# Optimization experiments

Measured on AMD Instinct MI355X. Metric: run time of the kernel, lower is better.

## Reference

```python
import jax, jax.numpy as jnp
import numpy as np

D_MODEL, N_LAYERS, D_INNER, D_STATE, D_CONV, DT_RANK, NUM_CLASSES = 256, 4, 512, 16, 4, 16, 10
B, L = 8, 1024


def setup_inputs() -> dict:
    key = jax.random.key(0)
    ks = jax.random.split(key, 16)
    s = 0.02
    inp = {}
    inp['x'] = jax.random.normal(ks[0], (B, L, 1), jnp.float32)
    inp['input_w'] = jax.random.normal(ks[1], (D_MODEL, 1), jnp.float32) * s
    inp['input_b'] = jnp.zeros((D_MODEL,), jnp.float32)
    inp['ln_w'] = jnp.ones((N_LAYERS, D_MODEL), jnp.float32)
    inp['ln_b'] = jnp.zeros((N_LAYERS, D_MODEL), jnp.float32)
    inp['in_proj_w'] = jax.random.normal(ks[2], (N_LAYERS, 2 * D_INNER, D_MODEL), jnp.float32) * s
    inp['in_proj_b'] = jnp.zeros((N_LAYERS, 2 * D_INNER), jnp.float32)
    inp['conv_w'] = jax.random.normal(ks[3], (N_LAYERS, D_INNER, 1, D_CONV), jnp.float32) * 0.2
    inp['conv_b'] = jnp.zeros((N_LAYERS, D_INNER), jnp.float32)
    inp['x_proj_w'] = jax.random.normal(ks[4], (N_LAYERS, DT_RANK + 2 * D_STATE, D_INNER), jnp.float32) * s
    inp['dt_proj_w'] = jax.random.normal(ks[5], (N_LAYERS, D_INNER, DT_RANK), jnp.float32) * s
    inp['dt_proj_b'] = jax.random.normal(ks[6], (N_LAYERS, D_INNER), jnp.float32) * 0.1 - 4.0  # small softplus(dt)
    # canonical S4D-real init: A = [1..d_state] repeated over d_inner
    A = jnp.tile(jnp.arange(1, D_STATE + 1, dtype=jnp.float32)[None, :], (D_INNER, 1))
    inp['A_log'] = jnp.tile(jnp.log(A)[None], (N_LAYERS, 1, 1))
    inp['D'] = jnp.ones((N_LAYERS, D_INNER), jnp.float32)
    inp['out_proj_w'] = jax.random.normal(ks[7], (N_LAYERS, D_MODEL, D_INNER), jnp.float32) * s
    inp['out_proj_b'] = jnp.zeros((N_LAYERS, D_MODEL), jnp.float32)
    inp['norm_w'] = jnp.ones((D_MODEL,), jnp.float32)
    inp['norm_b'] = jnp.zeros((D_MODEL,), jnp.float32)
    inp['cls_w'] = jax.random.normal(ks[8], (NUM_CLASSES, D_MODEL), jnp.float32) * s
    inp['cls_b'] = jnp.zeros((NUM_CLASSES,), jnp.float32)
    return inp


def _layernorm(x, w, b, eps=1e-5):
    mu = jnp.mean(x, axis=-1, keepdims=True)
    var = jnp.mean(jnp.square(x - mu), axis=-1, keepdims=True)
    return (x - mu) * jax.lax.rsqrt(var + eps) * w + b


def _causal_depthwise_conv(u, w, b):
    # u: (B, L, D_inner), w: (D_inner, 1, K), causal padding K-1
    out = jax.lax.conv_general_dilated(
        u.transpose(0, 2, 1), w, window_strides=(1,), padding=[(D_CONV - 1, 0)],
        feature_group_count=D_INNER, dimension_numbers=('NCH', 'OIH', 'NCH'))
    return out.transpose(0, 2, 1) + b


def _selective_scan(u, delta, A, Bm, Cm, Dp):
    # u, delta: (B,L,Din); Bm, Cm: (B,L,N); A: (Din,N); Dp: (Din,)
    def step(h, inp):
        d_t, B_t, C_t, u_t = inp                       # (B,Din),(B,N),(B,N),(B,Din)
        dA = jnp.exp(d_t[:, :, None] * A)              # (B,Din,N)
        dBu = d_t[:, :, None] * B_t[:, None, :] * u_t[:, :, None]
        h = dA * h + dBu
        y = jnp.einsum('bdn,bn->bd', h, C_t)
        return h, y
    h0 = jnp.zeros((u.shape[0], D_INNER, D_STATE), u.dtype)
    xs = (delta.transpose(1, 0, 2), Bm.transpose(1, 0, 2), Cm.transpose(1, 0, 2), u.transpose(1, 0, 2))
    _, ys = jax.lax.scan(step, h0, xs)                 # ys: (L,B,Din)
    return ys.transpose(1, 0, 2) + u * Dp


def _mamba_layer(x, ln_w, ln_b, ipw, ipb, cw, cb, xpw, dtw, dtb, A_log, Dp, opw, opb):
    h = _layernorm(x, ln_w, ln_b)
    xz = jnp.einsum('bld,ed->ble', h, ipw) + ipb       # (B,L,2*Din)
    u, res = jnp.split(xz, 2, axis=-1)
    u = jax.nn.silu(_causal_depthwise_conv(u, cw, cb))
    x_dbl = jnp.einsum('bld,ed->ble', u, xpw)          # (B,L,dt_rank+2N)
    dt, Bm, Cm = jnp.split(x_dbl, [DT_RANK, DT_RANK + D_STATE], axis=-1)
    delta = jax.nn.softplus(jnp.einsum('blr,dr->bld', dt, dtw) + dtb)
    A = -jnp.exp(A_log)
    y = _selective_scan(u, delta, A, Bm, Cm, Dp)
    y = y * jax.nn.silu(res)
    return x + jnp.einsum('ble,de->bld', y, opw) + opb


def reference(x, input_w, input_b, ln_w, ln_b, in_proj_w, in_proj_b, conv_w, conv_b,
              x_proj_w, dt_proj_w, dt_proj_b, A_log, D, out_proj_w, out_proj_b,
              norm_w, norm_b, cls_w, cls_b):
    h = jnp.einsum('blc,dc->bld', x, input_w) + input_b   # (B,L,D_MODEL)
    for i in range(N_LAYERS):
        h = _mamba_layer(h, ln_w[i], ln_b[i], in_proj_w[i], in_proj_b[i], conv_w[i], conv_b[i],
                         x_proj_w[i], dt_proj_w[i], dt_proj_b[i], A_log[i], D[i],
                         out_proj_w[i], out_proj_b[i])
    h = _layernorm(h, norm_w, norm_b)
    pooled = jnp.mean(h, axis=1)                          # (B, D_MODEL)
    return jnp.einsum('bd,cd->bc', pooled, cls_w) + cls_b
```

## Files before the change

kernel.cpp:

```cpp
#include <hip/hip_runtime.h>
#include <hip/hip_bf16.h>
#include <math.h>

#define DM 256
#define NL 4
#define DI 512
#define DS 16
#define DC 4
#define DR 16
#define NC 10
#define NB 8
#define LL 1024
#define MR (NB*LL)
#define NCHUNK 64
#define CLEN 16

typedef __attribute__((ext_vector_type(4))) float f32x4;
typedef __attribute__((ext_vector_type(8))) short short8;

extern "C" __device__ float __ocml_native_exp2_f32(float);
__device__ __forceinline__ float exp2_f(float x) { return __ocml_native_exp2_f32(x); }
#define L2E 1.442695040888963f

__device__ __forceinline__ float silu_f(float x) {
    return x * (1.0f / (1.0f + __expf(-x)));
}
__device__ __forceinline__ float bf2f(ushort v) {
    union { unsigned u; float f; } c; c.u = ((unsigned)v) << 16; return c.f;
}
__device__ __forceinline__ ushort f2bf(float f) {
    union { float f; unsigned u; } c; c.f = f;
    unsigned lsb = (c.u >> 16) & 1;
    return (ushort)((c.u + 0x7fffu + lsb) >> 16);
}
__device__ __forceinline__ void g2lds16(const void* g, void* l) {
    __builtin_amdgcn_global_load_lds((const __attribute__((address_space(1))) void*)g,
                                     (__attribute__((address_space(3))) void*)l, 16, 0, 0);
}

#define IPW_N (NL*2*DI*DM)
#define XPW_N (NL*64*DI)
#define OPW_N (NL*DM*DI)
__global__ __launch_bounds__(256) void convert_weights_kernel(
        const float* __restrict__ ipw, const float* __restrict__ xpw,
        const float* __restrict__ opw,
        ushort* __restrict__ ipw_b, ushort* __restrict__ xpw_b, ushort* __restrict__ opw_b) {
    int t = blockIdx.x * 256 + threadIdx.x;
    if (t < IPW_N) { ipw_b[t] = f2bf(ipw[t]); return; }
    t -= IPW_N;
    if (t < XPW_N) {
        int l = t >> 15, r = (t >> 9) & 63, k = t & 511;
        xpw_b[t] = (r < 48) ? f2bf(xpw[((size_t)l * 48 + r) * DI + k]) : (ushort)0;
        return;
    }
    t -= XPW_N;
    if (t < OPW_N) opw_b[t] = f2bf(opw[t]);
}

__global__ void input_proj_kernel(const float* __restrict__ x, const float* __restrict__ w,
                                  const float* __restrict__ b, float* __restrict__ h) {
    int t = blockIdx.x * 256 + threadIdx.x;
    if (t >= MR * DM) return;
    int d = t & (DM - 1);
    int m = t >> 8;
    h[t] = x[m] * w[d] + b[d];
}

__global__ __launch_bounds__(256) void layernorm_bf16_kernel(const float* __restrict__ in,
        const float* __restrict__ w, const float* __restrict__ b, ushort* __restrict__ out) {
    int row = blockIdx.x, t = threadIdx.x;
    float v = in[row * DM + t];
    float s = v, q = v * v;
#pragma unroll
    for (int o = 32; o >= 1; o >>= 1) { s += __shfl_xor(s, o); q += __shfl_xor(q, o); }
    __shared__ float red[8];
    int wid = t >> 6;
    if ((t & 63) == 0) { red[wid] = s; red[4 + wid] = q; }
    __syncthreads();
    s = red[0] + red[1] + red[2] + red[3];
    q = red[4] + red[5] + red[6] + red[7];
    float mu = s * (1.0f / DM);
    float var = q * (1.0f / DM) - mu * mu;
    float rs = rsqrtf(var + 1e-5f);
    out[row * DM + t] = f2bf((v - mu) * rs * w[t] + b[t]);
}

template<int BM, int BN, int WM, int WN, int MODE>
__global__ __launch_bounds__(256) void mfma_gemm_kernel(
        const ushort* __restrict__ A, int lda,
        const ushort* __restrict__ W,
        const float* __restrict__ bias,
        ushort* __restrict__ Cb, float* __restrict__ Cf, int ldc, int K) {
    constexpr int FM = BM / WM / 16;
    constexpr int FN = BN / WN / 16;
    __shared__ __align__(16) char smem[(BM + BN) * 128];
    const int tid = threadIdx.x;
    const int l = tid & 63, w = tid >> 6;
    const int wr = w / WN, wc = w % WN;
    const int bm = blockIdx.x * BM, bn = blockIdx.y * BN;
    const int ldw = K;

    f32x4 acc[FM][FN] = {};

    for (int k0 = 0; k0 < K; k0 += 64) {
#pragma unroll
        for (int i = 0; i < (BM * 128 / 16) / 256; i++) {
            int lin = (i * 256 + tid) * 16;
            int q = lin ^ (((lin >> 7) & 7) << 4);
            g2lds16(A + (size_t)(bm + (q >> 7)) * lda + k0 + ((q & 127) >> 1), smem + lin);
        }
#pragma unroll
        for (int i = 0; i < (BN * 128 / 16) / 256; i++) {
            int lin = (i * 256 + tid) * 16;
            int q = lin ^ (((lin >> 7) & 7) << 4);
            g2lds16(W + (size_t)(bn + (q >> 7)) * ldw + k0 + ((q & 127) >> 1),
                    smem + BM * 128 + lin);
        }
        __syncthreads();
        const int rl = l & 15;
        const int kb0 = ((l >> 4) << 3) * 2;
#pragma unroll
        for (int kk = 0; kk < 2; kk++) {
            short8 af[FM], bfr[FN];
#pragma unroll
            for (int m = 0; m < FM; m++) {
                int off = (wr * (BM / WM) + m * 16 + rl) * 128 + kk * 64 + kb0;
                off ^= ((off >> 7) & 7) << 4;
                af[m] = *(const short8*)(smem + off);
            }
#pragma unroll
            for (int n = 0; n < FN; n++) {
                int off = (wc * (BN / WN) + n * 16 + rl) * 128 + kk * 64 + kb0;
                off ^= ((off >> 7) & 7) << 4;
                bfr[n] = *(const short8*)(smem + BM * 128 + off);
            }
#pragma unroll
            for (int m = 0; m < FM; m++)
#pragma unroll
                for (int n = 0; n < FN; n++)
                    acc[m][n] = __builtin_amdgcn_mfma_f32_16x16x32_bf16(
                        af[m], bfr[n], acc[m][n], 0, 0, 0);
        }
        __syncthreads();
    }

    const int row0 = bm + wr * (BM / WM) + ((l >> 4) << 2);
    const int col0 = bn + wc * (BN / WN) + (l & 15);
#pragma unroll
    for (int m = 0; m < FM; m++) {
#pragma unroll
        for (int n = 0; n < FN; n++) {
            int col = col0 + n * 16;
            float bv = (MODE == 1) ? 0.f : bias[col];
#pragma unroll
            for (int r = 0; r < 4; r++) {
                size_t idx = (size_t)(row0 + m * 16 + r) * ldc + col;
                float v = acc[m][n][r];
                if (MODE == 0) Cb[idx] = f2bf(v + bv);
                else Cf[idx] = v;
            }
        }
    }
}

__global__ __launch_bounds__(256) void outproj_ln_kernel(
        const ushort* __restrict__ A,
        const ushort* __restrict__ W,
        const float* __restrict__ bias,
        float* __restrict__ hres,
        const float* __restrict__ lnw, const float* __restrict__ lnb,
        ushort* __restrict__ hln) {
    constexpr int K = DI;
    __shared__ __align__(16) char smem[(32 + 256) * 128];
    const int tid = threadIdx.x;
    const int l = tid & 63, w = tid >> 6;
    const int bm = blockIdx.x * 32;

    f32x4 acc[2][4] = {};

    for (int k0 = 0; k0 < K; k0 += 64) {
        {
            int lin = tid * 16;
            int q = lin ^ (((lin >> 7) & 7) << 4);
            g2lds16(A + (size_t)(bm + (q >> 7)) * K + k0 + ((q & 127) >> 1), smem + lin);
        }
#pragma unroll
        for (int i = 0; i < 8; i++) {
            int lin = (i * 256 + tid) * 16;
            int q = lin ^ (((lin >> 7) & 7) << 4);
            g2lds16(W + (size_t)(q >> 7) * K + k0 + ((q & 127) >> 1), smem + 32 * 128 + lin);
        }
        __syncthreads();
        const int rl = l & 15;
        const int kb0 = ((l >> 4) << 3) * 2;
#pragma unroll
        for (int kk = 0; kk < 2; kk++) {
            short8 af[2], bfr[4];
#pragma unroll
            for (int m = 0; m < 2; m++) {
                int off = (m * 16 + rl) * 128 + kk * 64 + kb0;
                off ^= ((off >> 7) & 7) << 4;
                af[m] = *(const short8*)(smem + off);
            }
#pragma unroll
            for (int n = 0; n < 4; n++) {
                int off = (w * 64 + n * 16 + rl) * 128 + kk * 64 + kb0;
                off ^= ((off >> 7) & 7) << 4;
                bfr[n] = *(const short8*)(smem + 32 * 128 + off);
            }
#pragma unroll
            for (int m = 0; m < 2; m++)
#pragma unroll
                for (int n = 0; n < 4; n++)
                    acc[m][n] = __builtin_amdgcn_mfma_f32_16x16x32_bf16(
                        af[m], bfr[n], acc[m][n], 0, 0, 0);
        }
        __syncthreads();
    }

    const int r0 = (l >> 4) << 2;
    const int col0 = w * 64 + (l & 15);
    float vv[2][4][4];
    float s[2][4], q[2][4];
#pragma unroll
    for (int m = 0; m < 2; m++)
#pragma unroll
        for (int r = 0; r < 4; r++) { s[m][r] = 0.f; q[m][r] = 0.f; }
#pragma unroll
    for (int m = 0; m < 2; m++) {
#pragma unroll
        for (int n = 0; n < 4; n++) {
            int col = col0 + n * 16;
            float bv = bias[col];
#pragma unroll
            for (int r = 0; r < 4; r++) {
                int row = bm + r0 + m * 16 + r;
                float x = acc[m][n][r] + bv + hres[(size_t)row * DM + col];
                vv[m][n][r] = x;
                s[m][r] += x;
                q[m][r] += x * x;
            }
        }
    }
#pragma unroll
    for (int o = 1; o < 16; o <<= 1) {
#pragma unroll
        for (int m = 0; m < 2; m++)
#pragma unroll
            for (int r = 0; r < 4; r++) {
                s[m][r] += __shfl_xor(s[m][r], o);
                q[m][r] += __shfl_xor(q[m][r], o);
            }
    }
    float* red  = (float*)smem;
    float* redq = red + 128;
    if ((l & 15) == 0) {
#pragma unroll
        for (int m = 0; m < 2; m++)
#pragma unroll
            for (int r = 0; r < 4; r++) {
                int rl2 = r0 + m * 16 + r;
                red[rl2 * 4 + w] = s[m][r];
                redq[rl2 * 4 + w] = q[m][r];
            }
    }
    __syncthreads();
#pragma unroll
    for (int m = 0; m < 2; m++) {
        float mu[4], rs[4];
#pragma unroll
        for (int r = 0; r < 4; r++) {
            int rl2 = r0 + m * 16 + r;
            float ts = red[rl2 * 4] + red[rl2 * 4 + 1] + red[rl2 * 4 + 2] + red[rl2 * 4 + 3];
            float tq = redq[rl2 * 4] + redq[rl2 * 4 + 1] + redq[rl2 * 4 + 2] + redq[rl2 * 4 + 3];
            mu[r] = ts * (1.0f / DM);
            float var = tq * (1.0f / DM) - mu[r] * mu[r];
            rs[r] = rsqrtf(var + 1e-5f);
        }
#pragma unroll
        for (int n = 0; n < 4; n++) {
            int col = col0 + n * 16;
            float lw = lnw[col], lb = lnb[col];
#pragma unroll
            for (int r = 0; r < 4; r++) {
                int row = bm + r0 + m * 16 + r;
                hres[(size_t)row * DM + col] = vv[m][n][r];
                hln[(size_t)row * DM + col] = f2bf((vv[m][n][r] - mu[r]) * rs[r] * lw + lb);
            }
        }
    }
}

__global__ __launch_bounds__(256) void conv_silu_kernel(const ushort* __restrict__ xz,
        const float* __restrict__ cw, const float* __restrict__ cb, ushort* __restrict__ u) {
    int t = blockIdx.x * 256 + threadIdx.x;
    int d8 = (t & 63) << 3;
    int m = t >> 6;
    int l = m & (LL - 1);
    const short8 zr = {0, 0, 0, 0, 0, 0, 0, 0};
    const size_t base = (size_t)m * 1024 + d8;
    short8 r3 = *(const short8*)(xz + base);
    short8 r2 = (l >= 1) ? *(const short8*)(xz + base - 1024) : zr;
    short8 r1 = (l >= 2) ? *(const short8*)(xz + base - 2048) : zr;
    short8 r0 = (l >= 3) ? *(const short8*)(xz + base - 3072) : zr;
    short8 o;
#pragma unroll
    for (int j = 0; j < 8; j++) {
        int d = d8 + j;
        float4 w4 = *reinterpret_cast<const float4*>(&cw[d * 4]);
        float a = cb[d] + w4.w * bf2f((ushort)r3[j]);
        a += w4.z * bf2f((ushort)r2[j]);
        a += w4.y * bf2f((ushort)r1[j]);
        a += w4.x * bf2f((ushort)r0[j]);
        o[j] = (short)f2bf(silu_f(a));
    }
    *(short8*)(u + (size_t)m * DI + d8) = o;
}

__global__ __launch_bounds__(256, 4) void scan_phase1_kernel(
        const ushort* __restrict__ u, const float* __restrict__ x_dbl,
        const float* __restrict__ A_log,
        const float* __restrict__ dtw, const float* __restrict__ dtb,
        float* __restrict__ sdv, float* __restrict__ Sbuf) {
    __shared__ __align__(16) float xs[CLEN * 64];
    const int tid = threadIdx.x;
    const int bc = blockIdx.x >> 1;
    const int d = ((blockIdx.x & 1) << 8) + tid;
    const int c = bc & (NCHUNK - 1);
    const int b = bc >> 6;
    const int m0 = b * LL + c * CLEN;
    *reinterpret_cast<float4*>(&xs[tid * 4]) =
        *reinterpret_cast<const float4*>(&x_dbl[(size_t)m0 * 64 + tid * 4]);

    float Aval[DS], h[DS], wreg[DR];
#pragma unroll
    for (int q = 0; q < 4; q++) {
        float4 a4 = *reinterpret_cast<const float4*>(&A_log[d * DS + q * 4]);
        Aval[q*4+0] = -__expf(a4.x) * L2E; Aval[q*4+1] = -__expf(a4.y) * L2E;
        Aval[q*4+2] = -__expf(a4.z) * L2E; Aval[q*4+3] = -__expf(a4.w) * L2E;
        float4 w4 = *reinterpret_cast<const float4*>(&dtw[d * DR + q * 4]);
        wreg[q*4] = w4.x; wreg[q*4+1] = w4.y; wreg[q*4+2] = w4.z; wreg[q*4+3] = w4.w;
    }
    float dbv = dtb[d];
#pragma unroll
    for (int n = 0; n < DS; n++) h[n] = 0.f;
    const ushort* up = u + (size_t)m0 * DI + d;
    float sd = 0.f;
    __syncthreads();
    float uv = bf2f(up[0]);
    for (int t = 0; t < CLEN; t++) {
        float uvn = (t + 1 < CLEN) ? bf2f(up[(size_t)(t + 1) * DI]) : 0.f;
        const float* xr = &xs[t * 64];
        float4 x0 = *reinterpret_cast<const float4*>(xr);
        float4 x1 = *reinterpret_cast<const float4*>(xr + 4);
        float4 x2 = *reinterpret_cast<const float4*>(xr + 8);
        float4 x3 = *reinterpret_cast<const float4*>(xr + 12);
        float4 B0 = *reinterpret_cast<const float4*>(xr + 16);
        float4 B1 = *reinterpret_cast<const float4*>(xr + 20);
        float4 B2 = *reinterpret_cast<const float4*>(xr + 24);
        float4 B3 = *reinterpret_cast<const float4*>(xr + 28);
        float p0 = dbv + wreg[0]*x0.x + wreg[1]*x0.y + wreg[2]*x0.z + wreg[3]*x0.w;
        float p1 = wreg[4]*x1.x + wreg[5]*x1.y + wreg[6]*x1.z + wreg[7]*x1.w;
        float p2 = wreg[8]*x2.x + wreg[9]*x2.y + wreg[10]*x2.z + wreg[11]*x2.w;
        float p3 = wreg[12]*x3.x + wreg[13]*x3.y + wreg[14]*x3.z + wreg[15]*x3.w;
        float z = (p0 + p1) + (p2 + p3);
        float dv = (z > 20.0f) ? z : __logf(1.0f + __expf(z));
        sd += dv;
        float du = dv * uv;
        h[0]  = exp2_f(dv*Aval[0])  * h[0]  + du * B0.x;
        h[1]  = exp2_f(dv*Aval[1])  * h[1]  + du * B0.y;
        h[2]  = exp2_f(dv*Aval[2])  * h[2]  + du * B0.z;
        h[3]  = exp2_f(dv*Aval[3])  * h[3]  + du * B0.w;
        h[4]  = exp2_f(dv*Aval[4])  * h[4]  + du * B1.x;
        h[5]  = exp2_f(dv*Aval[5])  * h[5]  + du * B1.y;
        h[6]  = exp2_f(dv*Aval[6])  * h[6]  + du * B1.z;
        h[7]  = exp2_f(dv*Aval[7])  * h[7]  + du * B1.w;
        h[8]  = exp2_f(dv*Aval[8])  * h[8]  + du * B2.x;
        h[9]  = exp2_f(dv*Aval[9])  * h[9]  + du * B2.y;
        h[10] = exp2_f(dv*Aval[10]) * h[10] + du * B2.z;
        h[11] = exp2_f(dv*Aval[11]) * h[11] + du * B2.w;
        h[12] = exp2_f(dv*Aval[12]) * h[12] + du * B3.x;
        h[13] = exp2_f(dv*Aval[13]) * h[13] + du * B3.y;
        h[14] = exp2_f(dv*Aval[14]) * h[14] + du * B3.z;
        h[15] = exp2_f(dv*Aval[15]) * h[15] + du * B3.w;
        uv = uvn;
    }
    size_t base = ((size_t)((b * NCHUNK + c) * DI + d)) * DS;
#pragma unroll
    for (int q = 0; q < 4; q++)
        *reinterpret_cast<float4*>(&Sbuf[base + q * 4]) =
            make_float4(h[q*4], h[q*4+1], h[q*4+2], h[q*4+3]);
    sdv[(b * NCHUNK + c) * DI + d] = sd;
}

__global__ __launch_bounds__(256) void scan_phase2_kernel(
        const float* __restrict__ sdv, const float* __restrict__ A_log,
        float* __restrict__ Sbuf) {
    int gid = blockIdx.x * 256 + threadIdx.x;
    int dn = gid & (DI * DS - 1);
    int b = gid >> 13;
    int n = dn & 15, d = dn >> 4;
    float Aval = -__expf(A_log[d * DS + n]) * L2E;
    size_t idx0 = (size_t)b * NCHUNK * DI * DS + dn;
    const size_t stride = (size_t)DI * DS;
    int sb0 = b * NCHUNK * DI + d;
    float h = 0.f;
    float S0[8], sd0[8];
#pragma unroll
    for (int j = 0; j < 8; j++) {
        S0[j] = Sbuf[idx0 + (size_t)j * stride];
        sd0[j] = sdv[sb0 + j * DI];
    }
    for (int g = 0; g < 8; g++) {
        float S1[8], sd1[8];
        if (g < 7) {
            int c1 = g * 8 + 8;
#pragma unroll
            for (int j = 0; j < 8; j++) {
                S1[j] = Sbuf[idx0 + (size_t)(c1 + j) * stride];
                sd1[j] = sdv[sb0 + (c1 + j) * DI];
            }
        } else {
#pragma unroll
            for (int j = 0; j < 8; j++) { S1[j] = 0.f; sd1[j] = 0.f; }
        }
#pragma unroll
        for (int j = 0; j < 8; j++) {
            float P = exp2_f(Aval * sd0[j]);
            Sbuf[idx0 + (size_t)(g * 8 + j) * stride] = h;
            h = P * h + S0[j];
        }
#pragma unroll
        for (int j = 0; j < 8; j++) { S0[j] = S1[j]; sd0[j] = sd1[j]; }
    }
}

__global__ __launch_bounds__(256, 4) void scan_phase3_kernel(
        const ushort* __restrict__ u, const float* __restrict__ x_dbl,
        const float* __restrict__ A_log,
        const float* __restrict__ dtw, const float* __restrict__ dtb,
        const float* __restrict__ Dp, const float* __restrict__ Sbuf,
        const ushort* __restrict__ xz, ushort* __restrict__ y) {
    __shared__ __align__(16) float xs[CLEN * 64];
    const int tid = threadIdx.x;
    const int bc = blockIdx.x >> 1;
    const int d = ((blockIdx.x & 1) << 8) + tid;
    const int c = bc & (NCHUNK - 1);
    const int b = bc >> 6;
    const int m0 = b * LL + c * CLEN;
    *reinterpret_cast<float4*>(&xs[tid * 4]) =
        *reinterpret_cast<const float4*>(&x_dbl[(size_t)m0 * 64 + tid * 4]);

    float Aval[DS], h[DS], wreg[DR];
#pragma unroll
    for (int q = 0; q < 4; q++) {
        float4 a4 = *reinterpret_cast<const float4*>(&A_log[d * DS + q * 4]);
        Aval[q*4+0] = -__expf(a4.x) * L2E; Aval[q*4+1] = -__expf(a4.y) * L2E;
        Aval[q*4+2] = -__expf(a4.z) * L2E; Aval[q*4+3] = -__expf(a4.w) * L2E;
        float4 w4 = *reinterpret_cast<const float4*>(&dtw[d * DR + q * 4]);
        wreg[q*4] = w4.x; wreg[q*4+1] = w4.y; wreg[q*4+2] = w4.z; wreg[q*4+3] = w4.w;
    }
    float dbv = dtb[d];
    size_t base = ((size_t)((b * NCHUNK + c) * DI + d)) * DS;
#pragma unroll
    for (int q = 0; q < 4; q++) {
        float4 h4 = *reinterpret_cast<const float4*>(&Sbuf[base + q * 4]);
        h[q*4] = h4.x; h[q*4+1] = h4.y; h[q*4+2] = h4.z; h[q*4+3] = h4.w;
    }
    float Dval = Dp[d];
    const ushort* up = u + (size_t)m0 * DI + d;
    const ushort* rp = xz + (size_t)m0 * 1024 + 512 + d;
    ushort* yp = y + (size_t)m0 * DI + d;
    __syncthreads();
    float uv = bf2f(up[0]);
    float rv = bf2f(rp[0]);
    for (int t = 0; t < CLEN; t++) {
        float uvn = 0.f, rvn = 0.f;
        if (t + 1 < CLEN) {
            uvn = bf2f(up[(size_t)(t + 1) * DI]);
            rvn = bf2f(rp[(size_t)(t + 1) * 1024]);
        }
        const float* xr = &xs[t * 64];
        float4 x0 = *reinterpret_cast<const float4*>(xr);
        float4 x1 = *reinterpret_cast<const float4*>(xr + 4);
        float4 x2 = *reinterpret_cast<const float4*>(xr + 8);
        float4 x3 = *reinterpret_cast<const float4*>(xr + 12);
        float4 B0 = *reinterpret_cast<const float4*>(xr + 16);
        float4 B1 = *reinterpret_cast<const float4*>(xr + 20);
        float4 B2 = *reinterpret_cast<const float4*>(xr + 24);
        float4 B3 = *reinterpret_cast<const float4*>(xr + 28);
        float4 C0 = *reinterpret_cast<const float4*>(xr + 32);
        float4 C1 = *reinterpret_cast<const float4*>(xr + 36);
        float4 C2 = *reinterpret_cast<const float4*>(xr + 40);
        float4 C3 = *reinterpret_cast<const float4*>(xr + 44);
        float p0 = dbv + wreg[0]*x0.x + wreg[1]*x0.y + wreg[2]*x0.z + wreg[3]*x0.w;
        float p1 = wreg[4]*x1.x + wreg[5]*x1.y + wreg[6]*x1.z + wreg[7]*x1.w;
        float p2 = wreg[8]*x2.x + wreg[9]*x2.y + wreg[10]*x2.z + wreg[11]*x2.w;
        float p3 = wreg[12]*x3.x + wreg[13]*x3.y + wreg[14]*x3.z + wreg[15]*x3.w;
        float z = (p0 + p1) + (p2 + p3);
        float dv = (z > 20.0f) ? z : __logf(1.0f + __expf(z));
        float du = dv * uv;
        float a0, a1, a2, a3;
        h[0]  = exp2_f(dv*Aval[0])  * h[0]  + du * B0.x;  a0  = h[0]  * C0.x;
        h[1]  = exp2_f(dv*Aval[1])  * h[1]  + du * B0.y;  a0 += h[1]  * C0.y;
        h[2]  = exp2_f(dv*Aval[2])  * h[2]  + du * B0.z;  a0 += h[2]  * C0.z;
        h[3]  = exp2_f(dv*Aval[3])  * h[3]  + du * B0.w;  a0 += h[3]  * C0.w;
        h[4]  = exp2_f(dv*Aval[4])  * h[4]  + du * B1.x;  a1  = h[4]  * C1.x;
        h[5]  = exp2_f(dv*Aval[5])  * h[5]  + du * B1.y;  a1 += h[5]  * C1.y;
        h[6]  = exp2_f(dv*Aval[6])  * h[6]  + du * B1.z;  a1 += h[6]  * C1.z;
        h[7]  = exp2_f(dv*Aval[7])  * h[7]  + du * B1.w;  a1 += h[7]  * C1.w;
        h[8]  = exp2_f(dv*Aval[8])  * h[8]  + du * B2.x;  a2  = h[8]  * C2.x;
        h[9]  = exp2_f(dv*Aval[9])  * h[9]  + du * B2.y;  a2 += h[9]  * C2.y;
        h[10] = exp2_f(dv*Aval[10]) * h[10] + du * B2.z;  a2 += h[10] * C2.z;
        h[11] = exp2_f(dv*Aval[11]) * h[11] + du * B2.w;  a2 += h[11] * C2.w;
        h[12] = exp2_f(dv*Aval[12]) * h[12] + du * B3.x;  a3  = h[12] * C3.x;
        h[13] = exp2_f(dv*Aval[13]) * h[13] + du * B3.y;  a3 += h[13] * C3.y;
        h[14] = exp2_f(dv*Aval[14]) * h[14] + du * B3.z;  a3 += h[14] * C3.z;
        h[15] = exp2_f(dv*Aval[15]) * h[15] + du * B3.w;  a3 += h[15] * C3.w;
        float acc = ((a0 + a1) + (a2 + a3)) + Dval * uv;
        yp[(size_t)t * DI] = f2bf(acc * silu_f(rv));
        uv = uvn; rv = rvn;
    }
}

__global__ __launch_bounds__(256) void pool_partial_kernel(const ushort* __restrict__ ln,
                                                           float* __restrict__ partial) {
    int bs = blockIdx.x;
    int b = bs >> 3, sl = bs & 7;
    int t = threadIdx.x;
    int l0 = sl * 128;
    float s = 0.f;
    for (int l = 0; l < 128; l++) s += bf2f(ln[(size_t)(b * LL + l0 + l) * DM + t]);
    partial[(bs << 8) + t] = s;
}

__global__ void cls_kernel(const float* __restrict__ partial, const float* __restrict__ cw,
                           const float* __restrict__ cb, float* __restrict__ out) {
    int t = threadIdx.x;
    if (t >= NB * NC) return;
    int b = t / NC, c = t % NC;
    float s = 0.f;
    for (int k = 0; k < DM; k++) {
        float p = 0.f;
#pragma unroll
        for (int sl = 0; sl < 8; sl++) p += partial[((b * 8 + sl) << 8) + k];
        s += p * cw[c * DM + k];
    }
    out[t] = cb[c] + s * (1.0f / LL);
}

extern "C" void kernel_launch(void* const* d_in, const int* in_sizes, int n_in,
                              void* d_out, int out_size, void* d_ws, size_t ws_size,
                              hipStream_t stream) {
    const float* x       = (const float*)d_in[0];
    const float* input_w = (const float*)d_in[1];
    const float* input_b = (const float*)d_in[2];
    const float* ln_w    = (const float*)d_in[3];
    const float* ln_b    = (const float*)d_in[4];
    const float* ipw     = (const float*)d_in[5];
    const float* ipb     = (const float*)d_in[6];
    const float* cw      = (const float*)d_in[7];
    const float* cb      = (const float*)d_in[8];
    const float* xpw     = (const float*)d_in[9];
    const float* dtw     = (const float*)d_in[10];
    const float* dtb     = (const float*)d_in[11];
    const float* A_log   = (const float*)d_in[12];
    const float* Dp      = (const float*)d_in[13];
    const float* opw     = (const float*)d_in[14];
    const float* opb     = (const float*)d_in[15];
    const float* norm_w  = (const float*)d_in[16];
    const float* norm_b  = (const float*)d_in[17];
    const float* cls_w   = (const float*)d_in[18];
    const float* cls_b   = (const float*)d_in[19];
    float* out = (float*)d_out;
    float* ws = (float*)d_ws;

    float*  hres   = ws;
    ushort* xz     = (ushort*)(hres + (size_t)MR * DM);
    ushort* ub     = xz + (size_t)MR * 1024;
    float*  x_dbl  = (float*)(ub + (size_t)MR * DI);
    float*  sdvb   = x_dbl + (size_t)MR * 64;
    float*  Sbuf   = sdvb + (size_t)NB * NCHUNK * DI;
    float*  partial= Sbuf + (size_t)NB * NCHUNK * DI * DS;
    ushort* ygate  = (ushort*)(partial + 64 * 256);
    ushort* hln    = ygate + (size_t)MR * DI;
    ushort* ipw_b  = hln + (size_t)MR * DM;
    ushort* xpw_b  = ipw_b + IPW_N;
    ushort* opw_b  = xpw_b + XPW_N;

    convert_weights_kernel<<<(IPW_N + XPW_N + OPW_N) / 256, 256, 0, stream>>>(
        ipw, xpw, opw, ipw_b, xpw_b, opw_b);
    input_proj_kernel<<<MR * DM / 256, 256, 0, stream>>>(x, input_w, input_b, hres);
    layernorm_bf16_kernel<<<MR, 256, 0, stream>>>(hres, ln_w, ln_b, hln);

    for (int i = 0; i < NL; i++) {
        mfma_gemm_kernel<128, 128, 2, 2, 0><<<dim3(MR / 128, 1024 / 128), 256, 0, stream>>>(
            hln, DM, ipw_b + (size_t)i * 2 * DI * DM, ipb + (size_t)i * 2 * DI,
            xz, nullptr, 1024, DM);
        conv_silu_kernel<<<MR * DI / 8 / 256, 256, 0, stream>>>(xz, cw + i * DI * DC, cb + i * DI, ub);
        mfma_gemm_kernel<64, 64, 4, 1, 1><<<dim3(MR / 64, 1), 256, 0, stream>>>(
            ub, DI, xpw_b + (size_t)i * 64 * DI, nullptr, nullptr, x_dbl, 64, DI);
        scan_phase1_kernel<<<NB * NCHUNK * DI / 256, 256, 0, stream>>>(
            ub, x_dbl, A_log + i * DI * DS, dtw + i * DI * DR, dtb + i * DI, sdvb, Sbuf);
        scan_phase2_kernel<<<NB * DI * DS / 256, 256, 0, stream>>>(
            sdvb, A_log + i * DI * DS, Sbuf);
        scan_phase3_kernel<<<NB * NCHUNK * DI / 256, 256, 0, stream>>>(
            ub, x_dbl, A_log + i * DI * DS, dtw + i * DI * DR, dtb + i * DI,
            Dp + i * DI, Sbuf, xz, ygate);
        const float* nlw = (i < NL - 1) ? (ln_w + (i + 1) * DM) : norm_w;
        const float* nlb = (i < NL - 1) ? (ln_b + (i + 1) * DM) : norm_b;
        outproj_ln_kernel<<<MR / 32, 256, 0, stream>>>(
            ygate, opw_b + (size_t)i * DM * DI, opb + (size_t)i * DM,
            hres, nlw, nlb, hln);
    }

    pool_partial_kernel<<<64, 256, 0, stream>>>(hln, partial);
    cls_kernel<<<1, 128, 0, stream>>>(partial, cls_w, cls_b, out);
}
```

Measured before the change: 444.3 us.

## Compute local chunk outputs in scan phase 1, apply carry-in correction in phase 3

Phase 1 now computes the within-chunk scan output (local y including the D*u term) and the running cumulative delta per timestep, writing both as fp32 buffers. Phase 3 no longer re-runs the recurrence. It adds the contribution of the carried-in state as exp(A*cumdelta)*h_in dotted with C, then applies the gating. This removes the duplicated softplus/dt projection and recurrence in phase 3, at the cost of extra global fp32 traffic for the cumd and yloc buffers (2 x MR x DI floats written and read).

```diff
diff --git a/kernel.cpp b/kernel.cpp
--- a/kernel.cpp
+++ b/kernel.cpp
@@ -321,7 +321,9 @@
         const ushort* __restrict__ u, const float* __restrict__ x_dbl,
         const float* __restrict__ A_log,
         const float* __restrict__ dtw, const float* __restrict__ dtb,
-        float* __restrict__ sdv, float* __restrict__ Sbuf) {
+        const float* __restrict__ Dp,
+        float* __restrict__ sdv, float* __restrict__ Sbuf,
+        float* __restrict__ cumd, float* __restrict__ yloc) {
     __shared__ __align__(16) float xs[CLEN * 64];
     const int tid = threadIdx.x;
     const int bc = blockIdx.x >> 1;
@@ -342,144 +344,17 @@
         wreg[q*4] = w4.x; wreg[q*4+1] = w4.y; wreg[q*4+2] = w4.z; wreg[q*4+3] = w4.w;
     }
     float dbv = dtb[d];
+    float Dval = Dp[d];
 #pragma unroll
     for (int n = 0; n < DS; n++) h[n] = 0.f;
     const ushort* up = u + (size_t)m0 * DI + d;
+    float* cp = cumd + (size_t)m0 * DI + d;
+    float* yp = yloc + (size_t)m0 * DI + d;
     float sd = 0.f;
     __syncthreads();
     float uv = bf2f(up[0]);
     for (int t = 0; t < CLEN; t++) {
         float uvn = (t + 1 < CLEN) ? bf2f(up[(size_t)(t + 1) * DI]) : 0.f;
-        const float* xr = &xs[t * 64];
-        float4 x0 = *reinterpret_cast<const float4*>(xr);
-        float4 x1 = *reinterpret_cast<const float4*>(xr + 4);
-        float4 x2 = *reinterpret_cast<const float4*>(xr + 8);
-        float4 x3 = *reinterpret_cast<const float4*>(xr + 12);
-        float4 B0 = *reinterpret_cast<const float4*>(xr + 16);
-        float4 B1 = *reinterpret_cast<const float4*>(xr + 20);
-        float4 B2 = *reinterpret_cast<const float4*>(xr + 24);
-        float4 B3 = *reinterpret_cast<const float4*>(xr + 28);
-        float p0 = dbv + wreg[0]*x0.x + wreg[1]*x0.y + wreg[2]*x0.z + wreg[3]*x0.w;
-        float p1 = wreg[4]*x1.x + wreg[5]*x1.y + wreg[6]*x1.z + wreg[7]*x1.w;
-        float p2 = wreg[8]*x2.x + wreg[9]*x2.y + wreg[10]*x2.z + wreg[11]*x2.w;
-        float p3 = wreg[12]*x3.x + wreg[13]*x3.y + wreg[14]*x3.z + wreg[15]*x3.w;
-        float z = (p0 + p1) + (p2 + p3);
-        float dv = (z > 20.0f) ? z : __logf(1.0f + __expf(z));
-        sd += dv;
-        float du = dv * uv;
-        h[0]  = exp2_f(dv*Aval[0])  * h[0]  + du * B0.x;
-        h[1]  = exp2_f(dv*Aval[1])  * h[1]  + du * B0.y;
-        h[2]  = exp2_f(dv*Aval[2])  * h[2]  + du * B0.z;
-        h[3]  = exp2_f(dv*Aval[3])  * h[3]  + du * B0.w;
-        h[4]  = exp2_f(dv*Aval[4])  * h[4]  + du * B1.x;
-        h[5]  = exp2_f(dv*Aval[5])  * h[5]  + du * B1.y;
-        h[6]  = exp2_f(dv*Aval[6])  * h[6]  + du * B1.z;
-        h[7]  = exp2_f(dv*Aval[7])  * h[7]  + du * B1.w;
-        h[8]  = exp2_f(dv*Aval[8])  * h[8]  + du * B2.x;
-        h[9]  = exp2_f(dv*Aval[9])  * h[9]  + du * B2.y;
-        h[10] = exp2_f(dv*Aval[10]) * h[10] + du * B2.z;
-        h[11] = exp2_f(dv*Aval[11]) * h[11] + du * B2.w;
-        h[12] = exp2_f(dv*Aval[12]) * h[12] + du * B3.x;
-        h[13] = exp2_f(dv*Aval[13]) * h[13] + du * B3.y;
-        h[14] = exp2_f(dv*Aval[14]) * h[14] + du * B3.z;
-        h[15] = exp2_f(dv*Aval[15]) * h[15] + du * B3.w;
-        uv = uvn;
-    }
-    size_t base = ((size_t)((b * NCHUNK + c) * DI + d)) * DS;
-#pragma unroll
-    for (int q = 0; q < 4; q++)
-        *reinterpret_cast<float4*>(&Sbuf[base + q * 4]) =
-            make_float4(h[q*4], h[q*4+1], h[q*4+2], h[q*4+3]);
-    sdv[(b * NCHUNK + c) * DI + d] = sd;
-}
-
-__global__ __launch_bounds__(256) void scan_phase2_kernel(
-        const float* __restrict__ sdv, const float* __restrict__ A_log,
-        float* __restrict__ Sbuf) {
-    int gid = blockIdx.x * 256 + threadIdx.x;
-    int dn = gid & (DI * DS - 1);
-    int b = gid >> 13;
-    int n = dn & 15, d = dn >> 4;
-    float Aval = -__expf(A_log[d * DS + n]) * L2E;
-    size_t idx0 = (size_t)b * NCHUNK * DI * DS + dn;
-    const size_t stride = (size_t)DI * DS;
-    int sb0 = b * NCHUNK * DI + d;
-    float h = 0.f;
-    float S0[8], sd0[8];
-#pragma unroll
-    for (int j = 0; j < 8; j++) {
-        S0[j] = Sbuf[idx0 + (size_t)j * stride];
-        sd0[j] = sdv[sb0 + j * DI];
-    }
-    for (int g = 0; g < 8; g++) {
-        float S1[8], sd1[8];
-        if (g < 7) {
-            int c1 = g * 8 + 8;
-#pragma unroll
-            for (int j = 0; j < 8; j++) {
-                S1[j] = Sbuf[idx0 + (size_t)(c1 + j) * stride];
-                sd1[j] = sdv[sb0 + (c1 + j) * DI];
-            }
-        } else {
-#pragma unroll
-            for (int j = 0; j < 8; j++) { S1[j] = 0.f; sd1[j] = 0.f; }
-        }
-#pragma unroll
-        for (int j = 0; j < 8; j++) {
-            float P = exp2_f(Aval * sd0[j]);
-            Sbuf[idx0 + (size_t)(g * 8 + j) * stride] = h;
-            h = P * h + S0[j];
-        }
-#pragma unroll
-        for (int j = 0; j < 8; j++) { S0[j] = S1[j]; sd0[j] = sd1[j]; }
-    }
-}
-
-__global__ __launch_bounds__(256, 4) void scan_phase3_kernel(
-        const ushort* __restrict__ u, const float* __restrict__ x_dbl,
-        const float* __restrict__ A_log,
-        const float* __restrict__ dtw, const float* __restrict__ dtb,
-        const float* __restrict__ Dp, const float* __restrict__ Sbuf,
-        const ushort* __restrict__ xz, ushort* __restrict__ y) {
-    __shared__ __align__(16) float xs[CLEN * 64];
-    const int tid = threadIdx.x;
-    const int bc = blockIdx.x >> 1;
-    const int d = ((blockIdx.x & 1) << 8) + tid;
-    const int c = bc & (NCHUNK - 1);
-    const int b = bc >> 6;
-    const int m0 = b * LL + c * CLEN;
-    *reinterpret_cast<float4*>(&xs[tid * 4]) =
-        *reinterpret_cast<const float4*>(&x_dbl[(size_t)m0 * 64 + tid * 4]);
-
-    float Aval[DS], h[DS], wreg[DR];
-#pragma unroll
-    for (int q = 0; q < 4; q++) {
-        float4 a4 = *reinterpret_cast<const float4*>(&A_log[d * DS + q * 4]);
-        Aval[q*4+0] = -__expf(a4.x) * L2E; Aval[q*4+1] = -__expf(a4.y) * L2E;
-        Aval[q*4+2] = -__expf(a4.z) * L2E; Aval[q*4+3] = -__expf(a4.w) * L2E;
-        float4 w4 = *reinterpret_cast<const float4*>(&dtw[d * DR + q * 4]);
-        wreg[q*4] = w4.x; wreg[q*4+1] = w4.y; wreg[q*4+2] = w4.z; wreg[q*4+3] = w4.w;
-    }
-    float dbv = dtb[d];
-    size_t base = ((size_t)((b * NCHUNK + c) * DI + d)) * DS;
-#pragma unroll
-    for (int q = 0; q < 4; q++) {
-        float4 h4 = *reinterpret_cast<const float4*>(&Sbuf[base + q * 4]);
-        h[q*4] = h4.x; h[q*4+1] = h4.y; h[q*4+2] = h4.z; h[q*4+3] = h4.w;
-    }
-    float Dval = Dp[d];
-    const ushort* up = u + (size_t)m0 * DI + d;
-    const ushort* rp = xz + (size_t)m0 * 1024 + 512 + d;
-    ushort* yp = y + (size_t)m0 * DI + d;
-    __syncthreads();
-    float uv = bf2f(up[0]);
-    float rv = bf2f(rp[0]);
-    for (int t = 0; t < CLEN; t++) {
-        float uvn = 0.f, rvn = 0.f;
-        if (t + 1 < CLEN) {
-            uvn = bf2f(up[(size_t)(t + 1) * DI]);
-            rvn = bf2f(rp[(size_t)(t + 1) * 1024]);
-        }
         const float* xr = &xs[t * 64];
         float4 x0 = *reinterpret_cast<const float4*>(xr);
         float4 x1 = *reinterpret_cast<const float4*>(xr + 4);
@@ -499,6 +374,8 @@
         float p3 = wreg[12]*x3.x + wreg[13]*x3.y + wreg[14]*x3.z + wreg[15]*x3.w;
         float z = (p0 + p1) + (p2 + p3);
         float dv = (z > 20.0f) ? z : __logf(1.0f + __expf(z));
+        sd += dv;
+        cp[(size_t)t * DI] = sd;
         float du = dv * uv;
         float a0, a1, a2, a3;
         h[0]  = exp2_f(dv*Aval[0])  * h[0]  + du * B0.x;  a0  = h[0]  * C0.x;
@@ -517,9 +394,129 @@
         h[13] = exp2_f(dv*Aval[13]) * h[13] + du * B3.y;  a3 += h[13] * C3.y;
         h[14] = exp2_f(dv*Aval[14]) * h[14] + du * B3.z;  a3 += h[14] * C3.z;
         h[15] = exp2_f(dv*Aval[15]) * h[15] + du * B3.w;  a3 += h[15] * C3.w;
-        float acc = ((a0 + a1) + (a2 + a3)) + Dval * uv;
-        yp[(size_t)t * DI] = f2bf(acc * silu_f(rv));
-        uv = uvn; rv = rvn;
+        yp[(size_t)t * DI] = ((a0 + a1) + (a2 + a3)) + Dval * uv;
+        uv = uvn;
+    }
+    size_t base = ((size_t)((b * NCHUNK + c) * DI + d)) * DS;
+#pragma unroll
+    for (int q = 0; q < 4; q++)
+        *reinterpret_cast<float4*>(&Sbuf[base + q * 4]) =
+            make_float4(h[q*4], h[q*4+1], h[q*4+2], h[q*4+3]);
+    sdv[(b * NCHUNK + c) * DI + d] = sd;
+}
+
+__global__ __launch_bounds__(256) void scan_phase2_kernel(
+        const float* __restrict__ sdv, const float* __restrict__ A_log,
+        float* __restrict__ Sbuf) {
+    int gid = blockIdx.x * 256 + threadIdx.x;
+    int dn = gid & (DI * DS - 1);
+    int b = gid >> 13;
+    int n = dn & 15, d = dn >> 4;
+    float Aval = -__expf(A_log[d * DS + n]) * L2E;
+    size_t idx0 = (size_t)b * NCHUNK * DI * DS + dn;
+    const size_t stride = (size_t)DI * DS;
+    int sb0 = b * NCHUNK * DI + d;
+    float h = 0.f;
+    float S0[8], sd0[8];
+#pragma unroll
+    for (int j = 0; j < 8; j++) {
+        S0[j] = Sbuf[idx0 + (size_t)j * stride];
+        sd0[j] = sdv[sb0 + j * DI];
+    }
+    for (int g = 0; g < 8; g++) {
+        float S1[8], sd1[8];
+        if (g < 7) {
+            int c1 = g * 8 + 8;
+#pragma unroll
+            for (int j = 0; j < 8; j++) {
+                S1[j] = Sbuf[idx0 + (size_t)(c1 + j) * stride];
+                sd1[j] = sdv[sb0 + (c1 + j) * DI];
+            }
+        } else {
+#pragma unroll
+            for (int j = 0; j < 8; j++) { S1[j] = 0.f; sd1[j] = 0.f; }
+        }
+#pragma unroll
+        for (int j = 0; j < 8; j++) {
+            float P = exp2_f(Aval * sd0[j]);
+            Sbuf[idx0 + (size_t)(g * 8 + j) * stride] = h;
+            h = P * h + S0[j];
+        }
+#pragma unroll
+        for (int j = 0; j < 8; j++) { S0[j] = S1[j]; sd0[j] = sd1[j]; }
+    }
+}
+
+__global__ __launch_bounds__(256, 4) void scan_phase3_kernel(
+        const float* __restrict__ cumd, const float* __restrict__ yloc,
+        const float* __restrict__ x_dbl, const float* __restrict__ A_log,
+        const float* __restrict__ Sbuf,
+        const ushort* __restrict__ xz, ushort* __restrict__ y) {
+    __shared__ __align__(16) float cs[CLEN * 16];
+    const int tid = threadIdx.x;
+    const int bc = blockIdx.x >> 1;
+    const int d = ((blockIdx.x & 1) << 8) + tid;
+    const int c = bc & (NCHUNK - 1);
+    const int b = bc >> 6;
+    const int m0 = b * LL + c * CLEN;
+    {
+        int tt = tid >> 4, k = tid & 15;
+        cs[tt * 16 + k] = x_dbl[(size_t)(m0 + tt) * 64 + 32 + k];
+    }
+    float Aval[DS], hi[DS];
+#pragma unroll
+    for (int q = 0; q < 4; q++) {
+        float4 a4 = *reinterpret_cast<const float4*>(&A_log[d * DS + q * 4]);
+        Aval[q*4+0] = -__expf(a4.x) * L2E; Aval[q*4+1] = -__expf(a4.y) * L2E;
+        Aval[q*4+2] = -__expf(a4.z) * L2E; Aval[q*4+3] = -__expf(a4.w) * L2E;
+    }
+    size_t base = ((size_t)((b * NCHUNK + c) * DI + d)) * DS;
+#pragma unroll
+    for (int q = 0; q < 4; q++) {
+        float4 h4 = *reinterpret_cast<const float4*>(&Sbuf[base + q * 4]);
+        hi[q*4] = h4.x; hi[q*4+1] = h4.y; hi[q*4+2] = h4.z; hi[q*4+3] = h4.w;
+    }
+    const float* cp = cumd + (size_t)m0 * DI + d;
+    const float* ylp = yloc + (size_t)m0 * DI + d;
+    const ushort* rp = xz + (size_t)m0 * 1024 + 512 + d;
+    ushort* yp = y + (size_t)m0 * DI + d;
+    __syncthreads();
+    float cd = cp[0];
+    float yl = ylp[0];
+    float rv = bf2f(rp[0]);
+#pragma unroll 4
+    for (int t = 0; t < CLEN; t++) {
+        float cdn = 0.f, yln = 0.f, rvn = 0.f;
+        if (t + 1 < CLEN) {
+            cdn = cp[(size_t)(t + 1) * DI];
+            yln = ylp[(size_t)(t + 1) * DI];
+            rvn = bf2f(rp[(size_t)(t + 1) * 1024]);
+        }
+        const float* cr = &cs[t * 16];
+        float4 C0 = *reinterpret_cast<const float4*>(cr);
+        float4 C1 = *reinterpret_cast<const float4*>(cr + 4);
+        float4 C2 = *reinterpret_cast<const float4*>(cr + 8);
+        float4 C3 = *reinterpret_cast<const float4*>(cr + 12);
+        float a0, a1, a2, a3;
+        a0  = exp2_f(Aval[0]  * cd) * hi[0]  * C0.x;
+        a0 += exp2_f(Aval[1]  * cd) * hi[1]  * C0.y;
+        a0 += exp2_f(Aval[2]  * cd) * hi[2]  * C0.z;
+        a0 += exp2_f(Aval[3]  * cd) * hi[3]  * C0.w;
+        a1  = exp2_f(Aval[4]  * cd) * hi[4]  * C1.x;
+        a1 += exp2_f(Aval[5]  * cd) * hi[5]  * C1.y;
+        a1 += exp2_f(Aval[6]  * cd) * hi[6]  * C1.z;
+        a1 += exp2_f(Aval[7]  * cd) * hi[7]  * C1.w;
+        a2  = exp2_f(Aval[8]  * cd) * hi[8]  * C2.x;
+        a2 += exp2_f(Aval[9]  * cd) * hi[9]  * C2.y;
+        a2 += exp2_f(Aval[10] * cd) * hi[10] * C2.z;
+        a2 += exp2_f(Aval[11] * cd) * hi[11] * C2.w;
+        a3  = exp2_f(Aval[12] * cd) * hi[12] * C3.x;
+        a3 += exp2_f(Aval[13] * cd) * hi[13] * C3.y;
+        a3 += exp2_f(Aval[14] * cd) * hi[14] * C3.z;
+        a3 += exp2_f(Aval[15] * cd) * hi[15] * C3.w;
+        float yv = yl + ((a0 + a1) + (a2 + a3));
+        yp[(size_t)t * DI] = f2bf(yv * silu_f(rv));
+        cd = cdn; yl = yln; rv = rvn;
     }
 }
 
@@ -587,6 +584,8 @@
     ushort* ipw_b  = hln + (size_t)MR * DM;
     ushort* xpw_b  = ipw_b + IPW_N;
     ushort* opw_b  = xpw_b + XPW_N;
+    float*  cumd   = (float*)(opw_b + OPW_N);
+    float*  yloc   = cumd + (size_t)MR * DI;
 
     convert_weights_kernel<<<(IPW_N + XPW_N + OPW_N) / 256, 256, 0, stream>>>(
         ipw, xpw, opw, ipw_b, xpw_b, opw_b);
@@ -600,13 +599,13 @@
         conv_silu_kernel<<<MR * DI / 8 / 256, 256, 0, stream>>>(xz, cw + i * DI * DC, cb + i * DI, ub);
         mfma_gemm_kernel<64, 64, 4, 1, 1><<<dim3(MR / 64, 1), 256, 0, stream>>>(
             ub, DI, xpw_b + (size_t)i * 64 * DI, nullptr, nullptr, x_dbl, 64, DI);
-        scan_phase1_kernel<<<NB * NCHUNK * DI / 256, 256, 0, stream>>>(
-            ub, x_dbl, A_log + i * DI * DS, dtw + i * DI * DR, dtb + i * DI, sdvb, Sbuf);
+        scan_phase1_kernel<<<NB * NCHUNK * 2, 256, 0, stream>>>(
+            ub, x_dbl, A_log + i * DI * DS, dtw + i * DI * DR, dtb + i * DI,
+            Dp + i * DI, sdvb, Sbuf, cumd, yloc);
         scan_phase2_kernel<<<NB * DI * DS / 256, 256, 0, stream>>>(
             sdvb, A_log + i * DI * DS, Sbuf);
-        scan_phase3_kernel<<<NB * NCHUNK * DI / 256, 256, 0, stream>>>(
-            ub, x_dbl, A_log + i * DI * DS, dtw + i * DI * DR, dtb + i * DI,
-            Dp + i * DI, Sbuf, xz, ygate);
+        scan_phase3_kernel<<<NB * NCHUNK * 2, 256, 0, stream>>>(
+            cumd, yloc, x_dbl, A_log + i * DI * DS, Sbuf, xz, ygate);
         const float* nlw = (i < NL - 1) ? (ln_w + (i + 1) * DM) : norm_w;
         const float* nlb = (i < NL - 1) ? (ln_b + (i + 1) * DM) : norm_b;
         outproj_ln_kernel<<<MR / 32, 256, 0, stream>>>(
```

Result: faster. 428.4 us (-3.6%).
